# Kernel optimization log

Hardware: AMD Instinct MI355X
Metric: run time of the kernel (lower is better)

Reference implementation:

```python
import jax, jax.numpy as jnp
import numpy as np

N, E, IDIM, HLD, H, ODIM = 40000, 640000, 64, 128, 2, 1


def setup_inputs() -> dict:
    key = jax.random.key(0)
    ks = jax.random.split(key, 16)
    g = lambda i, shape, scale=0.05: (jax.random.normal(ks[i], shape, jnp.float32) * scale)
    return {
        "x": jax.random.normal(ks[0], (N, IDIM), jnp.float32),
        "edgeIdx": jax.random.randint(ks[1], (2, E), 0, N, dtype=jnp.int32),
        "edgeAttr": jax.random.normal(ks[2], (E, 4), jnp.float32),  # unused by model (passed as None)
        "enc_w0": g(3, (IDIM, HLD)), "enc_b0": jnp.zeros((HLD,), jnp.float32),
        "enc_w1": g(4, (HLD, HLD)), "enc_b1": jnp.zeros((HLD,), jnp.float32),
        "gat0_W": g(5, (HLD, H * HLD)), "gat0_bl": jnp.zeros((H * HLD,), jnp.float32),
        "gat0_att": g(6, (H, HLD)), "gat0_bias": jnp.zeros((HLD,), jnp.float32),
        "gat1_W": g(7, (HLD, H * HLD)), "gat1_bl": jnp.zeros((H * HLD,), jnp.float32),
        "gat1_att": g(8, (H, HLD)), "gat1_bias": jnp.zeros((HLD,), jnp.float32),
        "dec_w0": g(9, (HLD, HLD)), "dec_b0": jnp.zeros((HLD,), jnp.float32),
        "dec_w1": g(10, (HLD, ODIM)), "dec_b1": jnp.zeros((ODIM,), jnp.float32),
    }


def _gatv2(x, src, dst, W, bl, att, bias):
    # GATv2Conv, share_weights=True, concat=False, add_self_loops=False
    h = (x @ W + bl).reshape(N, H, HLD)                      # [N,H,C]
    e = jax.nn.leaky_relu(h[src] + h[dst], negative_slope=0.2)  # [E,H,C]
    scores = jnp.einsum('ehc,hc->eh', e, att)                # [E,H]
    m = jax.ops.segment_max(scores, dst, num_segments=N)     # per-target max
    ex = jnp.exp(scores - m[dst])
    den = jax.ops.segment_sum(ex, dst, num_segments=N)
    alpha = ex / (den[dst] + 1e-16)                          # edge softmax [E,H]
    out = jax.ops.segment_sum(alpha[:, :, None] * h[src], dst, num_segments=N)
    return out.mean(axis=1) + bias, alpha


def reference(x, edgeIdx, edgeAttr, enc_w0, enc_b0, enc_w1, enc_b1,
              gat0_W, gat0_bl, gat0_att, gat0_bias,
              gat1_W, gat1_bl, gat1_att, gat1_bias,
              dec_w0, dec_b0, dec_w1, dec_b1):
    src, dst = edgeIdx[0], edgeIdx[1]
    h = jax.nn.silu(x @ enc_w0 + enc_b0)
    h = jax.nn.silu(h @ enc_w1 + enc_b1)
    h, alpha = _gatv2(h, src, dst, gat0_W, gat0_bl, gat0_att, gat0_bias)
    h = jax.nn.silu(h)
    h, alpha = _gatv2(h, src, dst, gat1_W, gat1_bl, gat1_att, gat1_bias)
    h = jax.nn.silu(h)
    h = h @ dec_w0 + dec_b0   # decode MLP has no activations
    h = h @ dec_w1 + dec_b1
    return h, alpha.mean(axis=1)
```

## Files before the change

kernel.cpp:

```cpp
#include <hip/hip_runtime.h>
#include <hip/hip_bf16.h>
#include <math.h>

#define NN 40000
#define EE 640000
#define IDIM 64
#define HLD 128
#define NH 2
#define HH 256

typedef __attribute__((ext_vector_type(8))) short short8;
typedef __attribute__((ext_vector_type(4))) float f32x4;

__device__ __forceinline__ float silu_f(float v) {
    return v / (1.0f + expf(-v));
}
__device__ __forceinline__ unsigned short f2bf(float f) {
    unsigned u = __float_as_uint(f);
    unsigned r = (u + 0x7FFFu + ((u >> 16) & 1u)) >> 16;
    return (unsigned short)r;
}
__device__ __forceinline__ float bf2f(unsigned short b) {
    return __uint_as_float((unsigned)b << 16);
}

__global__ void k_count(const int* __restrict__ dst, int* __restrict__ counts) {
    int e = blockIdx.x * 256 + threadIdx.x;
    if (e < EE) atomicAdd(&counts[dst[e]], 1);
}

__global__ void k_blocksum(const int* __restrict__ counts, int* __restrict__ bsum) {
    __shared__ int s[256];
    int t = threadIdx.x;
    int i = blockIdx.x * 256 + t;
    s[t] = (i < NN) ? counts[i] : 0;
    __syncthreads();
    for (int o = 128; o > 0; o >>= 1) {
        if (t < o) s[t] += s[t + o];
        __syncthreads();
    }
    if (t == 0) bsum[blockIdx.x] = s[0];
}

__global__ void k_scanb(int* __restrict__ bsum, int nb) {
    __shared__ int s[256];
    int t = threadIdx.x;
    int v = (t < nb) ? bsum[t] : 0;
    s[t] = v;
    __syncthreads();
    for (int o = 1; o < 256; o <<= 1) {
        int x = 0;
        if (t >= o) x = s[t - o];
        __syncthreads();
        s[t] += x;
        __syncthreads();
    }
    if (t < nb) bsum[t] = s[t] - v;
}

__global__ void k_scatter(const int* __restrict__ counts, const int* __restrict__ bsum,
                          int* __restrict__ offsets) {
    __shared__ int s[256];
    int t = threadIdx.x;
    int i = blockIdx.x * 256 + t;
    int v = (i < NN) ? counts[i] : 0;
    s[t] = v;
    __syncthreads();
    for (int o = 1; o < 256; o <<= 1) {
        int x = 0;
        if (t >= o) x = s[t - o];
        __syncthreads();
        s[t] += x;
        __syncthreads();
    }
    if (i < NN) offsets[i] = s[t] - v + bsum[blockIdx.x];
    if (i == 0) offsets[NN] = EE;
}

__global__ void k_fill(const int* __restrict__ dst, const int* __restrict__ src,
                       const int* __restrict__ offsets,
                       int* __restrict__ cursor, int* __restrict__ ebd,
                       int* __restrict__ ebs) {
    int e = blockIdx.x * 256 + threadIdx.x;
    if (e >= EE) return;
    int d = dst[e];
    int pos = offsets[d] + atomicAdd(&cursor[d], 1);
    ebd[pos] = e;
    ebs[pos] = src[e];
}

__global__ void k_cvtX(const float* __restrict__ in, unsigned short* __restrict__ out, int n4) {
    int i = blockIdx.x * 256 + threadIdx.x;
    if (i >= n4) return;
    float4 v = *(const float4*)(in + (size_t)i * 4);
    ushort4 o;
    o.x = f2bf(v.x); o.y = f2bf(v.y); o.z = f2bf(v.z); o.w = f2bf(v.w);
    *(ushort4*)(out + (size_t)i * 4) = o;
}

__global__ void k_cvtB(const float* __restrict__ W, unsigned short* __restrict__ out,
                       int K, int N) {
    int KB = K / 32;
    int total = (N / 16) * KB * 64;
    int idx = blockIdx.x * 256 + threadIdx.x;
    if (idx >= total) return;
    int lane = idx & 63;
    int t = idx >> 6;
    int kb = t % KB, nb = t / KB;
    int n = nb * 16 + (lane & 15);
    int kbase = kb * 32 + (lane >> 4) * 8;
    unsigned short tmp[8];
    #pragma unroll
    for (int j = 0; j < 8; j++) tmp[j] = f2bf(W[(size_t)(kbase + j) * N + n]);
    uint4 o;
    o.x = (unsigned)tmp[0] | ((unsigned)tmp[1] << 16);
    o.y = (unsigned)tmp[2] | ((unsigned)tmp[3] << 16);
    o.z = (unsigned)tmp[4] | ((unsigned)tmp[5] << 16);
    o.w = (unsigned)tmp[6] | ((unsigned)tmp[7] << 16);
    *(uint4*)(out + (size_t)idx * 8) = o;
}

template <int ACT, int KB, int NB>
__global__ __launch_bounds__(256) void k_mgemm(const unsigned short* __restrict__ A,
                                               const unsigned short* __restrict__ Bp,
                                               const float* __restrict__ bias,
                                               unsigned short* __restrict__ C) {
    const int K = KB * 32, N = NB * 16;
    int tid = threadIdx.x;
    int w = tid >> 6, lane = tid & 63;
    int m0 = blockIdx.x * 64 + w * 16;
    int lr = lane & 15, lk = lane >> 4;

    f32x4 acc[NB];
    #pragma unroll
    for (int nb = 0; nb < NB; nb++) acc[nb] = f32x4{0.f, 0.f, 0.f, 0.f};

    const unsigned short* Arow = A + (size_t)(m0 + lr) * K + lk * 8;
    #pragma unroll
    for (int kb = 0; kb < KB; kb++) {
        short8 af = *(const short8*)(Arow + kb * 32);
        const unsigned short* bp = Bp + ((size_t)kb * 64 + lane) * 8;
        #pragma unroll
        for (int nb = 0; nb < NB; nb++) {
            short8 bf = *(const short8*)(bp + (size_t)nb * KB * 64 * 8);
            acc[nb] = __builtin_amdgcn_mfma_f32_16x16x32_bf16(af, bf, acc[nb], 0, 0, 0);
        }
    }

    int row0 = m0 + lk * 4;
    #pragma unroll
    for (int nb = 0; nb < NB; nb++) {
        int col = nb * 16 + lr;
        float bcol = bias[col];
        #pragma unroll
        for (int r = 0; r < 4; r++) {
            float v = acc[nb][r] + bcol;
            if (ACT) v = silu_f(v);
            C[(size_t)(row0 + r) * N + col] = f2bf(v);
        }
    }
}

template <int WRITE_SCORES>
__global__ __launch_bounds__(256) void k_fused(const unsigned short* __restrict__ hproj,
                                               const float* __restrict__ att,
                                               const int* __restrict__ offsets,
                                               const int* __restrict__ ebs,
                                               const int* __restrict__ ebd,
                                               const float* __restrict__ bias,
                                               unsigned short* __restrict__ out,
                                               float* __restrict__ scores,
                                               float2* __restrict__ statMD) {
    int t = threadIdx.x;
    int wid = t >> 6, lane = t & 63;
    int n = blockIdx.x * 4 + wid;
    int h = lane >> 5;
    int cb = (lane & 31) * 4;
    int off = h * HLD + cb;
    const unsigned short* base = hproj + off;

    ushort4 hdb = *(const ushort4*)(base + (size_t)n * HH);
    float4 hd = make_float4(bf2f(hdb.x), bf2f(hdb.y), bf2f(hdb.z), bf2f(hdb.w));
    float4 at = *(const float4*)(att + off);
    int beg = offsets[n], end = offsets[n + 1];

    float m = -INFINITY, den = 0.0f;
    float4 acc = make_float4(0.f, 0.f, 0.f, 0.f);
    ushort4 hb0 = make_ushort4(0, 0, 0, 0);
    ushort4 hb1 = hb0;
    if (beg < end)     hb0 = *(const ushort4*)(base + (size_t)ebs[beg] * HH);
    if (beg + 1 < end) hb1 = *(const ushort4*)(base + (size_t)ebs[beg + 1] * HH);

    for (int i = beg; i < end; ++i) {
        float4 hs = make_float4(bf2f(hb0.x), bf2f(hb0.y), bf2f(hb0.z), bf2f(hb0.w));
        hb0 = hb1;
        if (i + 2 < end) hb1 = *(const ushort4*)(base + (size_t)ebs[i + 2] * HH);

        float v0 = hs.x + hd.x; v0 = (v0 > 0.f) ? v0 : 0.2f * v0;
        float v1 = hs.y + hd.y; v1 = (v1 > 0.f) ? v1 : 0.2f * v1;
        float v2 = hs.z + hd.z; v2 = (v2 > 0.f) ? v2 : 0.2f * v2;
        float v3 = hs.w + hd.w; v3 = (v3 > 0.f) ? v3 : 0.2f * v3;
        float p = v0 * at.x + v1 * at.y + v2 * at.z + v3 * at.w;
        #pragma unroll
        for (int o = 1; o < 32; o <<= 1) p += __shfl_xor(p, o, 64);

        if (WRITE_SCORES && (lane & 31) == 0)
            scores[(size_t)ebd[i] * 2 + h] = p;

        float mn = fmaxf(m, p);
        float sc = __expf(m - mn);
        float w  = __expf(p - mn);
        den   = den   * sc + w;
        acc.x = acc.x * sc + w * hs.x;
        acc.y = acc.y * sc + w * hs.y;
        acc.z = acc.z * sc + w * hs.z;
        acc.w = acc.w * sc + w * hs.w;
        m = mn;
    }

    float inv = (den > 0.f) ? 1.0f / (den + 1e-16f) : 0.0f;
    acc.x *= inv; acc.y *= inv; acc.z *= inv; acc.w *= inv;
    if (WRITE_SCORES && (lane & 31) == 0)
        statMD[(size_t)n * 2 + h] = make_float2(m, den);

    float o0 = 0.5f * (acc.x + __shfl_xor(acc.x, 32, 64));
    float o1 = 0.5f * (acc.y + __shfl_xor(acc.y, 32, 64));
    float o2 = 0.5f * (acc.z + __shfl_xor(acc.z, 32, 64));
    float o3 = 0.5f * (acc.w + __shfl_xor(acc.w, 32, 64));
    if (lane < 32) {
        float4 bv = *(const float4*)(bias + cb);
        ushort4 ov;
        ov.x = f2bf(silu_f(o0 + bv.x));
        ov.y = f2bf(silu_f(o1 + bv.y));
        ov.z = f2bf(silu_f(o2 + bv.z));
        ov.w = f2bf(silu_f(o3 + bv.w));
        *(ushort4*)(out + (size_t)n * HLD + cb) = ov;
    }
}

__global__ void k_alpha(const float* __restrict__ scores,
                        const int* __restrict__ dst,
                        const float2* __restrict__ statMD,
                        float* __restrict__ outAlpha) {
    int e = blockIdx.x * 256 + threadIdx.x;
    if (e >= EE) return;
    int d = dst[e];
    float2 md0 = statMD[(size_t)d * 2 + 0];
    float2 md1 = statMD[(size_t)d * 2 + 1];
    float s0 = scores[(size_t)e * 2 + 0];
    float s1 = scores[(size_t)e * 2 + 1];
    float a0 = __expf(s0 - md0.x) / (md0.y + 1e-16f);
    float a1 = __expf(s1 - md1.x) / (md1.y + 1e-16f);
    outAlpha[e] = 0.5f * (a0 + a1);
}

__global__ __launch_bounds__(256) void k_dec1(const unsigned short* __restrict__ hin,
                                              const float* __restrict__ w,
                                              const float* __restrict__ b,
                                              float* __restrict__ out) {
    int t = threadIdx.x;
    int row = blockIdx.x * 4 + (t >> 6);
    int lane = t & 63;
    if (row >= NN) return;
    const unsigned short* p = hin + (size_t)row * HLD;
    float sum = bf2f(p[lane]) * w[lane] + bf2f(p[lane + 64]) * w[lane + 64];
    #pragma unroll
    for (int o = 32; o > 0; o >>= 1) sum += __shfl_xor(sum, o, 64);
    if (lane == 0) out[row] = sum + b[0];
}

extern "C" void kernel_launch(void* const* d_in, const int* in_sizes, int n_in,
                              void* d_out, int out_size, void* d_ws, size_t ws_size,
                              hipStream_t stream) {
    const float* x       = (const float*)d_in[0];
    const int*   edgeIdx = (const int*)d_in[1];
    const float* enc_w0 = (const float*)d_in[3];
    const float* enc_b0 = (const float*)d_in[4];
    const float* enc_w1 = (const float*)d_in[5];
    const float* enc_b1 = (const float*)d_in[6];
    const float* gat_W[2]    = {(const float*)d_in[7],  (const float*)d_in[11]};
    const float* gat_bl[2]   = {(const float*)d_in[8],  (const float*)d_in[12]};
    const float* gat_att[2]  = {(const float*)d_in[9],  (const float*)d_in[13]};
    const float* gat_bias[2] = {(const float*)d_in[10], (const float*)d_in[14]};
    const float* dec_w0 = (const float*)d_in[15];
    const float* dec_b0 = (const float*)d_in[16];
    const float* dec_w1 = (const float*)d_in[17];
    const float* dec_b1 = (const float*)d_in[18];

    const int* esrc = edgeIdx;
    const int* edst = edgeIdx + EE;

    float* out = (float*)d_out;

    char* wsb = (char*)d_ws;
    float* scores  = (float*)wsb;
    float2* statMD = (float2*)(scores + (size_t)EE * 2);
    unsigned short* xbf   = (unsigned short*)(statMD + (size_t)NN * 2);
    unsigned short* hAbf  = xbf  + (size_t)NN * IDIM;
    unsigned short* hBbf  = hAbf + (size_t)NN * HLD;
    unsigned short* hproj = hBbf + (size_t)NN * HLD;
    unsigned short* wenc0p = hproj + (size_t)NN * HH;
    unsigned short* wenc1p = wenc0p + 64 * 128;
    unsigned short* wgat0p = wenc1p + 128 * 128;
    unsigned short* wgat1p = wgat0p + 128 * 256;
    unsigned short* wdec0p = wgat1p + 128 * 256;
    int* counts   = (int*)(wdec0p + 128 * 128);
    int* cursor   = counts + NN;
    int* offsets  = cursor + NN;
    int* bsum     = offsets + NN + 64;
    int* ebd      = bsum + 256;
    int* ebs      = ebd + EE;

    const int nb = (NN + 255) / 256;

    hipMemsetAsync(counts, 0, sizeof(int) * 2 * NN, stream);
    k_count<<<(EE + 255) / 256, 256, 0, stream>>>(edst, counts);
    k_blocksum<<<nb, 256, 0, stream>>>(counts, bsum);
    k_scanb<<<1, 256, 0, stream>>>(bsum, nb);
    k_scatter<<<nb, 256, 0, stream>>>(counts, bsum, offsets);
    k_fill<<<(EE + 255) / 256, 256, 0, stream>>>(edst, esrc, offsets, cursor, ebd, ebs);

    k_cvtX<<<(NN * IDIM / 4 + 255) / 256, 256, 0, stream>>>(x, xbf, NN * IDIM / 4);
    k_cvtB<<<(8 * 2 * 64 + 255) / 256, 256, 0, stream>>>(enc_w0, wenc0p, IDIM, HLD);
    k_cvtB<<<(8 * 4 * 64 + 255) / 256, 256, 0, stream>>>(enc_w1, wenc1p, HLD, HLD);
    k_cvtB<<<(16 * 4 * 64 + 255) / 256, 256, 0, stream>>>(gat_W[0], wgat0p, HLD, HH);
    k_cvtB<<<(16 * 4 * 64 + 255) / 256, 256, 0, stream>>>(gat_W[1], wgat1p, HLD, HH);
    k_cvtB<<<(8 * 4 * 64 + 255) / 256, 256, 0, stream>>>(dec_w0, wdec0p, HLD, HLD);

    k_mgemm<1, 2, 8><<<NN / 64, 256, 0, stream>>>(xbf, wenc0p, enc_b0, hAbf);
    k_mgemm<1, 4, 8><<<NN / 64, 256, 0, stream>>>(hAbf, wenc1p, enc_b1, hBbf);

    k_mgemm<0, 4, 16><<<NN / 64, 256, 0, stream>>>(hBbf, wgat0p, gat_bl[0], hproj);
    k_fused<0><<<NN / 4, 256, 0, stream>>>(hproj, gat_att[0], offsets, ebs, ebd,
                                           gat_bias[0], hAbf, nullptr, nullptr);

    k_mgemm<0, 4, 16><<<NN / 64, 256, 0, stream>>>(hAbf, wgat1p, gat_bl[1], hproj);
    k_fused<1><<<NN / 4, 256, 0, stream>>>(hproj, gat_att[1], offsets, ebs, ebd,
                                           gat_bias[1], hBbf, scores, statMD);
    k_alpha<<<(EE + 255) / 256, 256, 0, stream>>>(scores, edst, statMD, out + NN);

    k_mgemm<0, 4, 8><<<NN / 64, 256, 0, stream>>>(hBbf, wdec0p, dec_b0, hAbf);
    k_dec1<<<(NN + 3) / 4, 256, 0, stream>>>(hAbf, dec_w1, dec_b1, out);
}
```

Before: 472.8 us.

## Process four edges per wavefront iteration and drop online-softmax max tracking

Rewrites the fused GATv2 aggregation so each wavefront splits into four 16-lane groups that each handle one edge per iteration. Each lane now loads 16 bf16 channels with two uint4 loads, and the groups' partial sums are combined at the end with cross-lane shuffles. The running-max rescaling of the softmax is removed: raw exp(score) is accumulated directly and m is stored as 0, so the alpha kernel now reads the stats and scores with vector loads. This cuts per-edge shuffle and exp work and increases memory-level parallelism. In exchange, scores are no longer max-subtracted, so large scores could overflow exp, and registers per lane rise.

```diff
diff --git a/kernel.cpp b/kernel.cpp
--- a/kernel.cpp
+++ b/kernel.cpp
@@ -174,67 +174,119 @@
     int t = threadIdx.x;
     int wid = t >> 6, lane = t & 63;
     int n = blockIdx.x * 4 + wid;
-    int h = lane >> 5;
-    int cb = (lane & 31) * 4;
-    int off = h * HLD + cb;
-    const unsigned short* base = hproj + off;
-
-    ushort4 hdb = *(const ushort4*)(base + (size_t)n * HH);
-    float4 hd = make_float4(bf2f(hdb.x), bf2f(hdb.y), bf2f(hdb.z), bf2f(hdb.w));
-    float4 at = *(const float4*)(att + off);
+    int g = lane >> 4;
+    int s = lane & 15;
+    int h = s >> 3;
+    int cb = s * 16;
+
+    const unsigned* hp32 = (const unsigned*)hproj;
+
+    float hd[16], at[16];
+    {
+        const uint4* r = (const uint4*)(hp32 + (size_t)n * 128 + s * 8);
+        uint4 a0 = r[0], a1 = r[1];
+        unsigned dw[8] = {a0.x, a0.y, a0.z, a0.w, a1.x, a1.y, a1.z, a1.w};
+        #pragma unroll
+        for (int j = 0; j < 8; j++) {
+            hd[2*j]   = __uint_as_float(dw[j] << 16);
+            hd[2*j+1] = __uint_as_float(dw[j] & 0xffff0000u);
+        }
+    }
+    #pragma unroll
+    for (int j = 0; j < 16; j += 4) {
+        float4 a = *(const float4*)(att + cb + j);
+        at[j] = a.x; at[j+1] = a.y; at[j+2] = a.z; at[j+3] = a.w;
+    }
+
     int beg = offsets[n], end = offsets[n + 1];
 
-    float m = -INFINITY, den = 0.0f;
-    float4 acc = make_float4(0.f, 0.f, 0.f, 0.f);
-    ushort4 hb0 = make_ushort4(0, 0, 0, 0);
-    ushort4 hb1 = hb0;
-    if (beg < end)     hb0 = *(const ushort4*)(base + (size_t)ebs[beg] * HH);
-    if (beg + 1 < end) hb1 = *(const ushort4*)(base + (size_t)ebs[beg + 1] * HH);
-
-    for (int i = beg; i < end; ++i) {
-        float4 hs = make_float4(bf2f(hb0.x), bf2f(hb0.y), bf2f(hb0.z), bf2f(hb0.w));
-        hb0 = hb1;
-        if (i + 2 < end) hb1 = *(const ushort4*)(base + (size_t)ebs[i + 2] * HH);
-
-        float v0 = hs.x + hd.x; v0 = (v0 > 0.f) ? v0 : 0.2f * v0;
-        float v1 = hs.y + hd.y; v1 = (v1 > 0.f) ? v1 : 0.2f * v1;
-        float v2 = hs.z + hd.z; v2 = (v2 > 0.f) ? v2 : 0.2f * v2;
-        float v3 = hs.w + hd.w; v3 = (v3 > 0.f) ? v3 : 0.2f * v3;
-        float p = v0 * at.x + v1 * at.y + v2 * at.z + v3 * at.w;
-        #pragma unroll
-        for (int o = 1; o < 32; o <<= 1) p += __shfl_xor(p, o, 64);
-
-        if (WRITE_SCORES && (lane & 31) == 0)
-            scores[(size_t)ebd[i] * 2 + h] = p;
-
-        float mn = fmaxf(m, p);
-        float sc = __expf(m - mn);
-        float w  = __expf(p - mn);
-        den   = den   * sc + w;
-        acc.x = acc.x * sc + w * hs.x;
-        acc.y = acc.y * sc + w * hs.y;
-        acc.z = acc.z * sc + w * hs.z;
-        acc.w = acc.w * sc + w * hs.w;
-        m = mn;
-    }
+    float acc[16];
+    #pragma unroll
+    for (int j = 0; j < 16; j++) acc[j] = 0.f;
+    float den = 0.f;
+
+    uint4 c0 = make_uint4(0,0,0,0), c1 = c0;
+    if (beg + g < end) {
+        const uint4* r = (const uint4*)(hp32 + (size_t)ebs[beg + g] * 128 + s * 8);
+        c0 = r[0]; c1 = r[1];
+    }
+
+    for (int i = beg; i < end; i += 4) {
+        bool valid = (i + g) < end;
+        uint4 a0 = c0, a1 = c1;
+        int ni = i + 4 + g;
+        if (ni < end) {
+            const uint4* r = (const uint4*)(hp32 + (size_t)ebs[ni] * 128 + s * 8);
+            c0 = r[0]; c1 = r[1];
+        } else {
+            c0 = make_uint4(0,0,0,0); c1 = c0;
+        }
+
+        float hs[16];
+        {
+            unsigned dw[8] = {a0.x, a0.y, a0.z, a0.w, a1.x, a1.y, a1.z, a1.w};
+            #pragma unroll
+            for (int j = 0; j < 8; j++) {
+                hs[2*j]   = __uint_as_float(dw[j] << 16);
+                hs[2*j+1] = __uint_as_float(dw[j] & 0xffff0000u);
+            }
+        }
+        float p0 = 0.f, p1 = 0.f;
+        #pragma unroll
+        for (int j = 0; j < 16; j += 2) {
+            float v0 = hs[j] + hd[j];
+            v0 = fmaxf(v0, 0.2f * v0);
+            p0 = fmaf(v0, at[j], p0);
+            float v1 = hs[j+1] + hd[j+1];
+            v1 = fmaxf(v1, 0.2f * v1);
+            p1 = fmaf(v1, at[j+1], p1);
+        }
+        float p = p0 + p1;
+        p += __shfl_xor(p, 1, 64);
+        p += __shfl_xor(p, 2, 64);
+        p += __shfl_xor(p, 4, 64);
+        p = valid ? p : -1e30f;
+
+        if (WRITE_SCORES && valid && ((s & 7) == 0))
+            scores[(size_t)ebd[i + g] * 2 + h] = p;
+
+        float w = __expf(p);
+        den += w;
+        #pragma unroll
+        for (int j = 0; j < 16; j++) acc[j] = fmaf(w, hs[j], acc[j]);
+    }
+
+    #pragma unroll
+    for (int j = 0; j < 16; j++) {
+        acc[j] += __shfl_xor(acc[j], 16, 64);
+        acc[j] += __shfl_xor(acc[j], 32, 64);
+    }
+    den += __shfl_xor(den, 16, 64);
+    den += __shfl_xor(den, 32, 64);
+
+    if (WRITE_SCORES && (lane == 0 || lane == 8))
+        statMD[(size_t)n * 2 + h] = make_float2(0.f, den);
 
     float inv = (den > 0.f) ? 1.0f / (den + 1e-16f) : 0.0f;
-    acc.x *= inv; acc.y *= inv; acc.z *= inv; acc.w *= inv;
-    if (WRITE_SCORES && (lane & 31) == 0)
-        statMD[(size_t)n * 2 + h] = make_float2(m, den);
-
-    float o0 = 0.5f * (acc.x + __shfl_xor(acc.x, 32, 64));
-    float o1 = 0.5f * (acc.y + __shfl_xor(acc.y, 32, 64));
-    float o2 = 0.5f * (acc.z + __shfl_xor(acc.z, 32, 64));
-    float o3 = 0.5f * (acc.w + __shfl_xor(acc.w, 32, 64));
-    if (lane < 32) {
-        float4 bv = *(const float4*)(bias + cb);
-        ushort4 ov;
-        ov.x = f2bf(silu_f(o0 + bv.x));
-        ov.y = f2bf(silu_f(o1 + bv.y));
-        ov.z = f2bf(silu_f(o2 + bv.z));
-        ov.w = f2bf(silu_f(o3 + bv.w));
-        *(ushort4*)(out + (size_t)n * HLD + cb) = ov;
+    #pragma unroll
+    for (int j = 0; j < 16; j++) acc[j] *= inv;
+
+    float om[16];
+    #pragma unroll
+    for (int j = 0; j < 16; j++)
+        om[j] = 0.5f * (acc[j] + __shfl_xor(acc[j], 8, 64));
+
+    if (lane < 8) {
+        unsigned dwo[8];
+        #pragma unroll
+        for (int j = 0; j < 8; j++) {
+            float v0 = silu_f(om[2*j]   + bias[cb + 2*j]);
+            float v1 = silu_f(om[2*j+1] + bias[cb + 2*j + 1]);
+            dwo[j] = (unsigned)f2bf(v0) | ((unsigned)f2bf(v1) << 16);
+        }
+        unsigned* orow = (unsigned*)(out + (size_t)n * HLD + cb);
+        *(uint4*)orow       = make_uint4(dwo[0], dwo[1], dwo[2], dwo[3]);
+        *(uint4*)(orow + 4) = make_uint4(dwo[4], dwo[5], dwo[6], dwo[7]);
     }
 }
 
@@ -245,12 +297,10 @@
     int e = blockIdx.x * 256 + threadIdx.x;
     if (e >= EE) return;
     int d = dst[e];
-    float2 md0 = statMD[(size_t)d * 2 + 0];
-    float2 md1 = statMD[(size_t)d * 2 + 1];
-    float s0 = scores[(size_t)e * 2 + 0];
-    float s1 = scores[(size_t)e * 2 + 1];
-    float a0 = __expf(s0 - md0.x) / (md0.y + 1e-16f);
-    float a1 = __expf(s1 - md1.x) / (md1.y + 1e-16f);
+    float4 md = *(const float4*)&statMD[(size_t)d * 2];
+    float2 sc = *(const float2*)&scores[(size_t)e * 2];
+    float a0 = __expf(sc.x) / (md.y + 1e-16f);
+    float a1 = __expf(sc.y) / (md.w + 1e-16f);
     outAlpha[e] = 0.5f * (a0 + a1);
 }
 
```

Result: faster. 450.9 us (-4.6%).
